# Performance work log

Measured on AMD Instinct MI355X. Metric: run time of the kernel, lower is better.

The kernel has to match this reference:

```python
import jax, jax.numpy as jnp
import numpy as np

B, T, I, H = 128, 1024, 512, 1024

def setup_inputs() -> dict:
    key = jax.random.key(0)
    ks = jax.random.split(key, 7)
    stdv = 1.0 / np.sqrt(H)
    u = lambda k, shape: jax.random.uniform(k, shape, jnp.float32, -stdv, stdv)
    return {
        "x": jax.random.normal(ks[0], (B, T, I), jnp.float32),
        "lens": jax.random.randint(ks[1], (B,), 1, T + 1),
        "W": u(ks[2], (I, 4 * H)),
        "U": u(ks[3], (H, 4 * H)),
        "P": u(ks[4], (H, 2 * H)),
        "P_o": u(ks[5], (H, H)),
        "bias": u(ks[6], (4 * H,)),
    }

def reference(x, lens, W, U, P, P_o, bias):
    hs = P_o.shape[0]
    # Precompute input contribution to gates once: [B, T, 4H]
    xW = jnp.einsum('bti,ig->btg', x, W) + bias

    def step(c, g_x):
        gates = g_x + c @ U                      # [B, 4H] (gates use c_t, per source)
        peep = c @ P                             # [B, 2H]
        i_t = jax.nn.sigmoid(gates[:, :hs] + jnp.tanh(peep[:, :hs]))
        f_t = jax.nn.sigmoid(gates[:, hs:2 * hs] + jnp.tanh(peep[:, hs:]))
        g_t = jnp.tanh(gates[:, 2 * hs:3 * hs])
        c_new = f_t * c + i_t * g_t
        o_t = jax.nn.sigmoid(gates[:, 3 * hs:] + jnp.tanh(c_new @ P_o))
        h_t = o_t * jnp.tanh(c_new)
        return c_new, h_t

    c0 = jnp.zeros((x.shape[0], hs), x.dtype)
    _, h_seq = jax.lax.scan(step, c0, jnp.swapaxes(xW, 0, 1))  # h_seq: [T, B, H]
    h_seq = jnp.swapaxes(h_seq, 0, 1)                          # [B, T, H]
    batch_idx = jnp.arange(x.shape[0])
    return h_seq[batch_idx, lens - 1, :]
```

## Files before the change

### kernel.cpp

```cpp
#include <hip/hip_runtime.h>

typedef unsigned short u16;
typedef unsigned long long u64;
typedef __attribute__((ext_vector_type(8))) short bf16x8;
typedef __attribute__((ext_vector_type(4))) float f32x4;
typedef __attribute__((ext_vector_type(4))) u16 u16x4;


__device__ __forceinline__ float bf2f(u16 u) { return __uint_as_float(((unsigned)u) << 16); }
__device__ __forceinline__ u16 f2bf(float f) {
  unsigned u = __float_as_uint(f);
  u = (u + 0x7FFFu + ((u >> 16) & 1u)) >> 16;
  return (u16)u;
}
__device__ __forceinline__ float sigm_(float x) { return 1.0f / (1.0f + __expf(-x)); }
__device__ __forceinline__ float tanh_(float x) {
  float e = __expf(2.0f * fabsf(x));
  float r = 1.0f - 2.0f / (e + 1.0f);
  return copysignf(r, x);
}
__device__ __forceinline__ void g2l16(const void* g, void* l) {
  __builtin_amdgcn_global_load_lds(
      (const __attribute__((address_space(1))) void*)g,
      (__attribute__((address_space(3))) void*)l, 16, 0, 0);
}

__global__ __launch_bounds__(256) void k_cvt(const float* __restrict__ in,
                                             u16* __restrict__ out, int n) {
  int i = (blockIdx.x * 256 + threadIdx.x) * 4;
  if (i >= n) return;
  const float4 v = *(const float4*)(in + i);
  u16x4 o;
  o.x = f2bf(v.x); o.y = f2bf(v.y); o.z = f2bf(v.z); o.w = f2bf(v.w);
  *(u16x4*)(out + i) = o;
}

__global__ __launch_bounds__(256) void k_tr(const float* __restrict__ src, int ld,
                                            u16* __restrict__ out, int K) {
  __shared__ float tle[64][65];
  int j0 = blockIdx.x * 64, k0 = blockIdx.y * 64;
  int jc = threadIdx.x & 63, kq = threadIdx.x >> 6;
  #pragma unroll
  for (int p = 0; p < 16; ++p) {
    int kr = kq * 16 + p;
    tle[jc][kr] = src[(size_t)(k0 + kr) * ld + j0 + jc];
  }
  __syncthreads();
  #pragma unroll
  for (int p = 0; p < 16; ++p) {
    int jr = kq * 16 + p;
    out[(size_t)(j0 + jr) * K + k0 + jc] = f2bf(tle[jr][jc]);
  }
}

__global__ __launch_bounds__(256) void k_gemm(const u16* __restrict__ A,
                                              const u16* __restrict__ Bt,
                                              const float* __restrict__ bias,
                                              u16* __restrict__ xw) {
  __shared__ u16 lds[16384];
  const int Kd = 512;
  int n0 = blockIdx.x * 128, m0 = blockIdx.y * 128;
  int tid = threadIdx.x, lane = tid & 63, wave = tid >> 6;
  int wm = (wave >> 1) * 64, wn = (wave & 1) * 64;
  int l15 = lane & 15, lk8 = (lane >> 4) * 8;
  f32x4 acc[4][4];
  #pragma unroll
  for (int i = 0; i < 4; ++i)
    #pragma unroll
    for (int j = 0; j < 4; ++j) {
      acc[i][j][0] = 0.f; acc[i][j][1] = 0.f; acc[i][j][2] = 0.f; acc[i][j][3] = 0.f;
    }
  for (int k0 = 0; k0 < Kd; k0 += 64) {
    #pragma unroll
    for (int p = 0; p < 8; ++p) {
      int c = p * 256 + tid;
      int ldsbase = (c - lane) * 16;
      int row = (c & 1023) >> 3, colb = (c & 7) * 16;
      const char* g;
      if (c < 1024) g = (const char*)A  + ((size_t)(m0 + row) * Kd + k0) * 2 + colb;
      else          g = (const char*)Bt + ((size_t)(n0 + row) * Kd + k0) * 2 + colb;
      g2l16(g, (char*)lds + ldsbase);
    }
    __syncthreads();
    #pragma unroll
    for (int kk = 0; kk < 2; ++kk) {
      bf16x8 af[4], bfr[4];
      #pragma unroll
      for (int mf = 0; mf < 4; ++mf)
        af[mf] = *(const bf16x8*)&lds[(wm + mf * 16 + l15) * 64 + kk * 32 + lk8];
      #pragma unroll
      for (int nf = 0; nf < 4; ++nf)
        bfr[nf] = *(const bf16x8*)&lds[8192 + (wn + nf * 16 + l15) * 64 + kk * 32 + lk8];
      #pragma unroll
      for (int mf = 0; mf < 4; ++mf)
        #pragma unroll
        for (int nf = 0; nf < 4; ++nf)
          acc[mf][nf] = __builtin_amdgcn_mfma_f32_16x16x32_bf16(af[mf], bfr[nf], acc[mf][nf], 0, 0, 0);
    }
    __syncthreads();
  }
  int rbase = (lane >> 4) * 4;
  #pragma unroll
  for (int mf = 0; mf < 4; ++mf)
    #pragma unroll
    for (int nf = 0; nf < 4; ++nf) {
      int n = n0 + wn + nf * 16 + l15;
      float bv = bias[n];
      size_t mrow = (size_t)(m0 + wm + mf * 16 + rbase);
      #pragma unroll
      for (int r = 0; r < 4; ++r)
        xw[(mrow + r) * 3072 + n] = f2bf(acc[mf][nf][r] + bv);
    }
}

__device__ __forceinline__ void gbar_nf(unsigned* bar, unsigned phase, int bid) {
  __syncthreads();
  if (threadIdx.x == 0) {
    unsigned* gc = bar + (bid >> 5) * 32;
    unsigned v = __hip_atomic_fetch_add(gc, 1u, __ATOMIC_RELAXED, __HIP_MEMORY_SCOPE_AGENT) + 1;
    if (v == 32u * phase)
      __hip_atomic_fetch_add(bar + 512, 1u, __ATOMIC_RELAXED, __HIP_MEMORY_SCOPE_AGENT);
    while (__hip_atomic_load(bar + 512, __ATOMIC_RELAXED, __HIP_MEMORY_SCOPE_AGENT) < 8u * phase)
      __builtin_amdgcn_s_sleep(2);
  }
  __syncthreads();
}

__global__ __launch_bounds__(320) void k_persist(
    u16* __restrict__ cb, const u16* __restrict__ wcat, const u16* __restrict__ xw,
    const int* __restrict__ lens, float* __restrict__ sp, float* __restrict__ sn,
    unsigned* __restrict__ bar) {
  __shared__ __align__(16) char smem[98304];
  char* Ab = smem;
  float* sgl = (float*)(smem + 65536);

  const int bid = blockIdx.x;
  const int jb = bid & 63, rb = bid >> 6;
  const int tid = threadIdx.x;
  const int lane = tid & 63, wave = tid >> 6;
  const int l15 = lane & 15, lhi = lane >> 4;
  const int swz = (l15 & 7) << 4;

  const u16* brow = wcat + ((size_t)(wave * 1024 + jb * 16 + l15)) * 1024 + lhi * 8;
  bf16x8 breg[32];
  #pragma unroll
  for (int kf = 0; kf < 32; ++kf)
    breg[kf] = *(const bf16x8*)(brow + kf * 32);

  const int erow = tid >> 3, ejj = (tid & 7) * 2;
  const int eb = rb * 32 + erow;
  const int ej0 = jb * 16 + ejj;
  const int mylen = (tid < 256) ? lens[eb] : 0;
  float c0 = 0.f, c1 = 0.f;

  #pragma unroll 1
  for (int t = 0; t < 1024; ++t) {
    const u64* asrc = (const u64*)((const char*)cb + (size_t)(t & 1) * 262144 +
                                   (size_t)rb * 65536);
    u16* cbout = cb + (size_t)((t + 1) & 1) * 131072;

    unsigned xg0 = 0, xg1 = 0, xg2 = 0;
    if (tid < 256) {
      const u16* xr = xw + ((size_t)eb * 1024 + t) * 3072 + ej0;
      xg0 = *(const unsigned*)xr;
      xg1 = *(const unsigned*)(xr + 1024);
      xg2 = *(const unsigned*)(xr + 2048);
    }

    u64 av[26];
    #pragma unroll
    for (int i = 0; i < 26; ++i) {
      int c = i * 320 + tid;
      if (c < 8192)
        av[i] = __hip_atomic_load(asrc + c, __ATOMIC_RELAXED, __HIP_MEMORY_SCOPE_AGENT);
    }
    #pragma unroll
    for (int i = 0; i < 26; ++i) {
      int c = i * 320 + tid;
      if (c < 8192) {
        int row = c >> 8, col8 = c & 255;
        *(u64*)(Ab + row * 2048 + ((col8 * 8) ^ ((row & 7) << 4))) = av[i];
      }
    }
    __syncthreads();

    f32x4 acc0 = {0.f, 0.f, 0.f, 0.f}, acc1 = {0.f, 0.f, 0.f, 0.f};
    #pragma unroll
    for (int kf = 0; kf < 32; ++kf) {
      int koff = (kf * 64 + lhi * 16) ^ swz;
      bf16x8 a0 = *(const bf16x8*)(Ab + l15 * 2048 + koff);
      bf16x8 a1 = *(const bf16x8*)(Ab + (16 + l15) * 2048 + koff);
      acc0 = __builtin_amdgcn_mfma_f32_16x16x32_bf16(a0, breg[kf], acc0, 0, 0, 0);
      acc1 = __builtin_amdgcn_mfma_f32_16x16x32_bf16(a1, breg[kf], acc1, 0, 0, 0);
    }

    *(f32x4*)&sgl[(wave * 16 + l15) * 36 + lhi * 4] = acc0;
    *(f32x4*)&sgl[(wave * 16 + l15) * 36 + 16 + lhi * 4] = acc1;
    __syncthreads();

    if (tid < 256) {
      float ci[2] = {c0, c1};
      float cn2[2];
      u16 nb2[2];
      unsigned xg[3] = {xg0, xg1, xg2};
      #pragma unroll
      for (int e = 0; e < 2; ++e) {
        int col = ejj + e;
        float gi = sgl[(0 * 16 + col) * 36 + erow] + bf2f((u16)(xg[0] >> (e * 16)));
        float gf = sgl[(1 * 16 + col) * 36 + erow] + bf2f((u16)(xg[1] >> (e * 16)));
        float gg = sgl[(2 * 16 + col) * 36 + erow] + bf2f((u16)(xg[2] >> (e * 16)));
        float pi = sgl[(3 * 16 + col) * 36 + erow];
        float pf = sgl[(4 * 16 + col) * 36 + erow];
        float it = sigm_(gi + tanh_(pi));
        float ft = sigm_(gf + tanh_(pf));
        float gt = tanh_(gg);
        float cn = ft * ci[e] + it * gt;
        cn2[e] = cn;
        nb2[e] = f2bf(cn);
      }
      c0 = cn2[0]; c1 = cn2[1];
      __hip_atomic_store((unsigned*)(cbout + (size_t)eb * 1024 + ej0),
                         (unsigned)nb2[0] | ((unsigned)nb2[1] << 16),
                         __ATOMIC_RELAXED, __HIP_MEMORY_SCOPE_AGENT);
      if (t == mylen - 1) {
        *(float2*)(sp + (size_t)eb * 1024 + ej0) = make_float2(ci[0], ci[1]);
        *(float2*)(sn + (size_t)eb * 1024 + ej0) = make_float2(cn2[0], cn2[1]);
      }
    }

    gbar_nf(bar, (unsigned)(t + 1), bid);
  }
}

__global__ __launch_bounds__(256) void k_final(
    const int* __restrict__ lens, const float* __restrict__ x,
    const float* __restrict__ W, const float* __restrict__ U,
    const float* __restrict__ Po, const float* __restrict__ bias,
    const float* __restrict__ sp, const float* __restrict__ sn,
    float* __restrict__ out) {
  __shared__ float scp[1024], scn[1024], sx[512];
  int b = blockIdx.x, tid = threadIdx.x;
  int t = lens[b] - 1;
  for (int k = tid; k < 1024; k += 256) {
    scp[k] = sp[b * 1024 + k];
    scn[k] = sn[b * 1024 + k];
  }
  for (int k = tid; k < 512; k += 256)
    sx[k] = x[(size_t)(b * 1024 + t) * 512 + k];
  __syncthreads();
  for (int j = tid; j < 1024; j += 256) {
    float au = 0.f, ap = 0.f, ax = 0.f;
    for (int k = 0; k < 1024; ++k) {
      au = fmaf(scp[k], U[(size_t)k * 4096 + 3072 + j], au);
      ap = fmaf(scn[k], Po[(size_t)k * 1024 + j], ap);
    }
    for (int k = 0; k < 512; ++k)
      ax = fmaf(sx[k], W[(size_t)k * 4096 + 3072 + j], ax);
    float go = ax + bias[3072 + j] + au;
    float o = sigm_(go + tanh_(ap));
    out[b * 1024 + j] = o * tanh_(scn[j]);
  }
}

extern "C" void kernel_launch(void* const* d_in, const int* in_sizes, int n_in,
                              void* d_out, int out_size, void* d_ws, size_t ws_size,
                              hipStream_t stream) {
  const float* x    = (const float*)d_in[0];
  const int*   lens = (const int*)d_in[1];
  const float* W    = (const float*)d_in[2];
  const float* U    = (const float*)d_in[3];
  const float* P    = (const float*)d_in[4];
  const float* Po   = (const float*)d_in[5];
  const float* bias = (const float*)d_in[6];
  float* out = (float*)d_out;
  char* ws = (char*)d_ws;

  u16*      xw   = (u16*)(ws);
  u16*      xbf  = (u16*)(ws + 805306368LL);
  u16*      wt   = (u16*)(ws + 939524096LL);
  u16*      wcat = (u16*)(ws + 943718400LL);
  u16*      cbp  = (u16*)(ws + 954204160LL);
  float*    sp   = (float*)(ws + 954728448LL);
  float*    sn   = (float*)(ws + 955252736LL);
  unsigned* bar  = (unsigned*)(ws + 955777024LL);

  hipMemsetAsync(cbp, 0, 262144, stream);
  hipMemsetAsync(bar, 0, 4096, stream);

  k_cvt<<<65536, 256, 0, stream>>>(x, xbf, 67108864);
  k_tr<<<dim3(48, 8), 256, 0, stream>>>(W, 4096, wt, 512);
  k_tr<<<dim3(48, 16), 256, 0, stream>>>(U, 4096, wcat, 1024);
  k_tr<<<dim3(32, 16), 256, 0, stream>>>(P, 2048, wcat + (size_t)3072 * 1024, 1024);
  k_gemm<<<dim3(24, 1024), 256, 0, stream>>>(xbf, wt, bias, xw);

  void* ka[] = {(void*)&cbp, (void*)&wcat, (void*)&xw, (void*)&lens,
                (void*)&sp, (void*)&sn, (void*)&bar};
  hipLaunchCooperativeKernel((const void*)k_persist, dim3(256), dim3(320), ka, 0, stream);

  k_final<<<128, 256, 0, stream>>>(lens, x, W, U, Po, bias, sp, sn, out);
}
```

Measured before the change: 8.165 ms.

## Scope grid barrier per row-block, retile xW layout, split MFMA accumulators

The global barrier is replaced with one barrier per batch row-block. Each group of 64 blocks that shares a batch slice syncs only with itself, since the recurrence on c is independent across batch rows. The precomputed xW gates are stored in a time-major, block-tiled layout so each step's gate loads are contiguous per block. The MFMA k-loop also uses two independent accumulator chains to shorten the dependency chain. The risks are the larger barrier array and a scatter-style store in the xW GEMM epilogue.

Measured after the change: 6.771 ms. 1.21x faster.

```diff
diff --git a/kernel.cpp b/kernel.cpp
--- a/kernel.cpp
+++ b/kernel.cpp
@@ -106,22 +106,29 @@
     for (int nf = 0; nf < 4; ++nf) {
       int n = n0 + wn + nf * 16 + l15;
       float bv = bias[n];
-      size_t mrow = (size_t)(m0 + wm + mf * 16 + rbase);
-      #pragma unroll
-      for (int r = 0; r < 4; ++r)
-        xw[(mrow + r) * 3072 + n] = f2bf(acc[mf][nf][r] + bv);
-    }
-}
-
-__device__ __forceinline__ void gbar_nf(unsigned* bar, unsigned phase, int bid) {
+      int g = n >> 10, j = n & 1023;
+      int jbp = j >> 4, col = j & 15;
+      #pragma unroll
+      for (int r = 0; r < 4; ++r) {
+        int m = m0 + wm + mf * 16 + rbase + r;
+        int b = m >> 10, t = m & 1023;
+        xw[(((size_t)t * 64 + jbp) * 128 + b) * 48 + g * 16 + col] =
+            f2bf(acc[mf][nf][r] + bv);
+      }
+    }
+}
+
+__device__ __forceinline__ void gbar_rb(unsigned* bar, unsigned phase, int jb, int rb) {
   __syncthreads();
   if (threadIdx.x == 0) {
-    unsigned* gc = bar + (bid >> 5) * 32;
+    unsigned* barg = bar + rb * 256;
+    unsigned* gc = barg + (jb >> 5) * 32;
+    unsigned* master = barg + 128;
     unsigned v = __hip_atomic_fetch_add(gc, 1u, __ATOMIC_RELAXED, __HIP_MEMORY_SCOPE_AGENT) + 1;
     if (v == 32u * phase)
-      __hip_atomic_fetch_add(bar + 512, 1u, __ATOMIC_RELAXED, __HIP_MEMORY_SCOPE_AGENT);
-    while (__hip_atomic_load(bar + 512, __ATOMIC_RELAXED, __HIP_MEMORY_SCOPE_AGENT) < 8u * phase)
-      __builtin_amdgcn_s_sleep(2);
+      __hip_atomic_fetch_add(master, 1u, __ATOMIC_RELAXED, __HIP_MEMORY_SCOPE_AGENT);
+    while (__hip_atomic_load(master, __ATOMIC_RELAXED, __HIP_MEMORY_SCOPE_AGENT) < 2u * phase)
+      __builtin_amdgcn_s_sleep(1);
   }
   __syncthreads();
 }
@@ -161,10 +168,10 @@
 
     unsigned xg0 = 0, xg1 = 0, xg2 = 0;
     if (tid < 256) {
-      const u16* xr = xw + ((size_t)eb * 1024 + t) * 3072 + ej0;
-      xg0 = *(const unsigned*)xr;
-      xg1 = *(const unsigned*)(xr + 1024);
-      xg2 = *(const unsigned*)(xr + 2048);
+      const u16* xr = xw + (((size_t)t * 64 + jb) * 128 + eb) * 48 + ejj;
+      xg0 = *(const unsigned*)(xr);
+      xg1 = *(const unsigned*)(xr + 16);
+      xg2 = *(const unsigned*)(xr + 32);
     }
 
     u64 av[26];
@@ -185,14 +192,22 @@
     __syncthreads();
 
     f32x4 acc0 = {0.f, 0.f, 0.f, 0.f}, acc1 = {0.f, 0.f, 0.f, 0.f};
-    #pragma unroll
-    for (int kf = 0; kf < 32; ++kf) {
-      int koff = (kf * 64 + lhi * 16) ^ swz;
-      bf16x8 a0 = *(const bf16x8*)(Ab + l15 * 2048 + koff);
-      bf16x8 a1 = *(const bf16x8*)(Ab + (16 + l15) * 2048 + koff);
+    f32x4 acc2 = {0.f, 0.f, 0.f, 0.f}, acc3 = {0.f, 0.f, 0.f, 0.f};
+    #pragma unroll
+    for (int kf = 0; kf < 32; kf += 2) {
+      int koffA = (kf * 64 + lhi * 16) ^ swz;
+      int koffB = ((kf + 1) * 64 + lhi * 16) ^ swz;
+      bf16x8 a0 = *(const bf16x8*)(Ab + l15 * 2048 + koffA);
+      bf16x8 a1 = *(const bf16x8*)(Ab + (16 + l15) * 2048 + koffA);
+      bf16x8 b0 = *(const bf16x8*)(Ab + l15 * 2048 + koffB);
+      bf16x8 b1 = *(const bf16x8*)(Ab + (16 + l15) * 2048 + koffB);
       acc0 = __builtin_amdgcn_mfma_f32_16x16x32_bf16(a0, breg[kf], acc0, 0, 0, 0);
       acc1 = __builtin_amdgcn_mfma_f32_16x16x32_bf16(a1, breg[kf], acc1, 0, 0, 0);
-    }
+      acc2 = __builtin_amdgcn_mfma_f32_16x16x32_bf16(b0, breg[kf + 1], acc2, 0, 0, 0);
+      acc3 = __builtin_amdgcn_mfma_f32_16x16x32_bf16(b1, breg[kf + 1], acc3, 0, 0, 0);
+    }
+    acc0[0] += acc2[0]; acc0[1] += acc2[1]; acc0[2] += acc2[2]; acc0[3] += acc2[3];
+    acc1[0] += acc3[0]; acc1[1] += acc3[1]; acc1[2] += acc3[2]; acc1[3] += acc3[3];
 
     *(f32x4*)&sgl[(wave * 16 + l15) * 36 + lhi * 4] = acc0;
     *(f32x4*)&sgl[(wave * 16 + l15) * 36 + 16 + lhi * 4] = acc1;
@@ -228,7 +243,7 @@
       }
     }
 
-    gbar_nf(bar, (unsigned)(t + 1), bid);
+    gbar_rb(bar, (unsigned)(t + 1), jb, rb);
   }
 }
 
```
